# Optimization experiments

Measured on AMD Instinct MI355X. Metric: run time of the kernel, lower is better.

## Reference

```python
import jax, jax.numpy as jnp
import numpy as np

BATCH, SEQ_LEN, HIDDEN, N_TYPES = 8, 1024, 256, 4
MAX_SPAN = 12


def _span_indices(seq_len: int, max_span_length: int):
    # Enumerate (start, end) pairs in the exact order of the original triple loop:
    # start ascending, end ascending within [start, min(start+max_span, seq_len)).
    starts, ends = [], []
    for s in range(seq_len):
        for e in range(s, min(s + max_span_length, seq_len)):
            starts.append(s)
            ends.append(e)
    return np.asarray(starts, np.int32), np.asarray(ends, np.int32)


def setup_inputs() -> dict:
    key = jax.random.key(0)
    k1, k2, k3 = jax.random.split(key, 3)
    hidden_states = jax.random.normal(k1, (BATCH, SEQ_LEN, HIDDEN), dtype=jnp.float32)
    # Stacked nn.Linear(2H -> H) weights for each entity type: W[t] has shape [H, 2H]
    W = jax.random.normal(k2, (N_TYPES, HIDDEN, 2 * HIDDEN), dtype=jnp.float32) * 0.02
    b = jax.random.normal(k3, (N_TYPES, HIDDEN), dtype=jnp.float32) * 0.02
    return {"hidden_states": hidden_states, "W": W, "b": b, "max_span_length": MAX_SPAN}


def reference(hidden_states, W, b, max_span_length):
    B, S, H = hidden_states.shape
    T = W.shape[0]
    start_idx, end_idx = _span_indices(S, int(max_span_length))  # [N]
    N = start_idx.shape[0]
    h_start = hidden_states[:, start_idx, :]          # [B, N, H]
    h_end = hidden_states[:, end_idx, :]              # [B, N, H]
    cat = jnp.concatenate([h_start, h_end], axis=-1)  # [B, N, 2H]
    # Per-type linear: y = x @ W_t^T + b_t, entity type is the innermost stacking axis
    out = jnp.einsum('bnc,thc->bnth', cat, W) + b     # [B, N, T, H]
    return out.reshape(B, N * T, H)
```

## Files before the change

kernel.cpp:

```cpp
#include <hip/hip_runtime.h>
#include <hip/hip_bf16.h>
#include <cstdint>
#include <cstddef>

#define BATCH   8
#define SEQLEN  1024
#define HIDDEN  256
#define NTYPES  4
#define NSPAN   12222
#define NFULL   12156
#define NPAD    12288
#define KDIM    512
#define NCOL    1024

typedef __bf16 bf16x8 __attribute__((ext_vector_type(8)));
typedef float  f32x4  __attribute__((ext_vector_type(4)));

#define AS1 __attribute__((address_space(1)))
#define AS3 __attribute__((address_space(3)))

__device__ __forceinline__ void load16(const __bf16* g, __bf16* l) {
    __builtin_amdgcn_global_load_lds((AS1 const void*)g, (AS3 void*)l, 16, 0, 0);
}

__global__ void cvt_bf16(const float* __restrict__ src, __bf16* __restrict__ dst, int n) {
    int i = (blockIdx.x * 256 + threadIdx.x) * 4;
    if (i + 3 < n) {
        float4 f = *(const float4*)(src + i);
        struct alignas(8) B4 { __bf16 a, b, c, d; };
        B4 v;
        v.a = (__bf16)f.x; v.b = (__bf16)f.y; v.c = (__bf16)f.z; v.d = (__bf16)f.w;
        *(B4*)(dst + i) = v;
    }
}

__global__ void mk_idx(int* __restrict__ sA, int* __restrict__ eA) {
    int n = blockIdx.x * 256 + threadIdx.x;
    if (n >= NPAD) return;
    int s = 0, e = 0;
    if (n < NFULL) {
        s = n / 12;
        e = s + (n - s * 12);
    } else if (n < NSPAN) {
        int r = n - NFULL;
        s = SEQLEN - 11;
        int cnt = 11;
        while (r >= cnt) { r -= cnt; --cnt; ++s; }
        e = s + r;
    }
    sA[n] = s; eA[n] = e;
}

__global__ __launch_bounds__(256) void span_gemm(
    const __bf16* __restrict__ Hbf,
    const __bf16* __restrict__ Wbf,
    const int*    __restrict__ idxS,
    const int*    __restrict__ idxE,
    const float*  __restrict__ bias,
    float*        __restrict__ out)
{
    __shared__ alignas(16) __bf16 As[128 * 32];
    __shared__ alignas(16) __bf16 Bs[128 * 32];

    const int tid  = threadIdx.x;
    const int wave = tid >> 6;
    const int lane = tid & 63;
    const int wm   = (wave >> 1) * 64;
    const int wn   = (wave & 1) * 64;
    const int lr   = lane & 15;
    const int lq   = lane >> 4;

    const int j0 = blockIdx.x * 128;
    const int n0 = blockIdx.y * 128;
    const int b  = blockIdx.z;

    const int l0  = wave * 1024 + lane * 8;
    const int l1  = l0 + 512;
    const int mm0 = l0 >> 5, kk0 = l0 & 31;
    const int mm1 = l1 >> 5, kk1 = l1 & 31;

    const int s0 = idxS[n0 + mm0], e0 = idxE[n0 + mm0];
    const int s1 = idxS[n0 + mm1], e1 = idxE[n0 + mm1];

    const __bf16* hb = Hbf + (size_t)b * (SEQLEN * HIDDEN);
    const __bf16* w0 = Wbf + (size_t)(j0 + mm0) * KDIM + kk0;
    const __bf16* w1 = Wbf + (size_t)(j0 + mm1) * KDIM + kk1;

    f32x4 acc[4][4];
#pragma unroll
    for (int i = 0; i < 4; ++i)
#pragma unroll
        for (int j = 0; j < 4; ++j)
            acc[i][j] = (f32x4){0.f, 0.f, 0.f, 0.f};

    for (int half = 0; half < 2; ++half) {
        const __bf16* a0  = hb + (half ? e0 : s0) * HIDDEN + kk0;
        const __bf16* a1  = hb + (half ? e1 : s1) * HIDDEN + kk1;
        const __bf16* wb0 = w0 + half * HIDDEN;
        const __bf16* wb1 = w1 + half * HIDDEN;

        for (int ks = 0; ks < 8; ++ks) {
            const int c0 = ks * 32;
            __syncthreads();
            load16(a0  + c0, &As[l0]);
            load16(a1  + c0, &As[l1]);
            load16(wb0 + c0, &Bs[l0]);
            load16(wb1 + c0, &Bs[l1]);
            __syncthreads();

            bf16x8 af[4], bfv[4];
#pragma unroll
            for (int mi = 0; mi < 4; ++mi)
                af[mi] = *(const bf16x8*)(As + (wm + mi * 16 + lr) * 32 + lq * 8);
#pragma unroll
            for (int ni = 0; ni < 4; ++ni)
                bfv[ni] = *(const bf16x8*)(Bs + (wn + ni * 16 + lr) * 32 + lq * 8);
#pragma unroll
            for (int mi = 0; mi < 4; ++mi)
#pragma unroll
                for (int ni = 0; ni < 4; ++ni)
                    acc[mi][ni] = __builtin_amdgcn_mfma_f32_16x16x32_bf16(
                        af[mi], bfv[ni], acc[mi][ni], 0, 0, 0);
        }
    }

    float bv[4];
#pragma unroll
    for (int ni = 0; ni < 4; ++ni) bv[ni] = bias[j0 + wn + ni * 16 + lr];

    const size_t obase = (size_t)b * NSPAN * NCOL;
#pragma unroll
    for (int mi = 0; mi < 4; ++mi) {
#pragma unroll
        for (int r = 0; r < 4; ++r) {
            const int n = n0 + wm + mi * 16 + lq * 4 + r;
            if (n < NSPAN) {
                float* op = out + obase + (size_t)n * NCOL + (j0 + wn + lr);
#pragma unroll
                for (int ni = 0; ni < 4; ++ni)
                    op[ni * 16] = acc[mi][ni][r] + bv[ni];
            }
        }
    }
}

extern "C" void kernel_launch(void* const* d_in, const int* in_sizes, int n_in,
                              void* d_out, int out_size, void* d_ws, size_t ws_size,
                              hipStream_t stream) {
    const float* hid  = (const float*)d_in[0];
    const float* W    = (const float*)d_in[1];
    const float* bias = (const float*)d_in[2];
    float* out = (float*)d_out;

    char* ws = (char*)d_ws;
    __bf16* Wbf = (__bf16*)ws;
    __bf16* Hbf = (__bf16*)(ws + (size_t)1048576);
    int* idxS = (int*)(ws + (size_t)(1048576 + 4194304));
    int* idxE = idxS + NPAD;

    cvt_bf16<<<512,  256, 0, stream>>>(W,   Wbf, NCOL * KDIM);
    cvt_bf16<<<2048, 256, 0, stream>>>(hid, Hbf, BATCH * SEQLEN * HIDDEN);
    mk_idx<<<NPAD / 256, 256, 0, stream>>>(idxS, idxE);
    span_gemm<<<dim3(8, 96, BATCH), 256, 0, stream>>>(Hbf, Wbf, idxS, idxE, bias, out);
}
```

Measured before the change: 465.5 us.

## Factor span linear into per-token start/end projections plus gather-add

Instead of running a GEMM over all spans with a concatenated K of 512, the linear is split into start and end halves, each computed once per token (8192 rows) into an fp32 workspace PQ. A second kernel then gathers P[start] + Q[end] + bias for each span and writes the output. This removes roughly 12x redundant matmul FLOPs, at the cost of an extra 64MB fp32 intermediate written and reread. The workspace must be large enough to hold it.

```diff
diff --git a/kernel.cpp b/kernel.cpp
--- a/kernel.cpp
+++ b/kernel.cpp
@@ -6,12 +6,11 @@
 #define BATCH   8
 #define SEQLEN  1024
 #define HIDDEN  256
-#define NTYPES  4
 #define NSPAN   12222
 #define NFULL   12156
-#define NPAD    12288
 #define KDIM    512
 #define NCOL    1024
+#define NROW    8192
 
 typedef __bf16 bf16x8 __attribute__((ext_vector_type(8)));
 typedef float  f32x4  __attribute__((ext_vector_type(4)));
@@ -34,30 +33,10 @@
     }
 }
 
-__global__ void mk_idx(int* __restrict__ sA, int* __restrict__ eA) {
-    int n = blockIdx.x * 256 + threadIdx.x;
-    if (n >= NPAD) return;
-    int s = 0, e = 0;
-    if (n < NFULL) {
-        s = n / 12;
-        e = s + (n - s * 12);
-    } else if (n < NSPAN) {
-        int r = n - NFULL;
-        s = SEQLEN - 11;
-        int cnt = 11;
-        while (r >= cnt) { r -= cnt; --cnt; ++s; }
-        e = s + r;
-    }
-    sA[n] = s; eA[n] = e;
-}
-
-__global__ __launch_bounds__(256) void span_gemm(
+__global__ __launch_bounds__(256) void pq_gemm(
     const __bf16* __restrict__ Hbf,
     const __bf16* __restrict__ Wbf,
-    const int*    __restrict__ idxS,
-    const int*    __restrict__ idxE,
-    const float*  __restrict__ bias,
-    float*        __restrict__ out)
+    float*        __restrict__ PQ)
 {
     __shared__ alignas(16) __bf16 As[128 * 32];
     __shared__ alignas(16) __bf16 Bs[128 * 32];
@@ -70,21 +49,19 @@
     const int lr   = lane & 15;
     const int lq   = lane >> 4;
 
-    const int j0 = blockIdx.x * 128;
-    const int n0 = blockIdx.y * 128;
-    const int b  = blockIdx.z;
+    const int j0   = blockIdx.x * 128;
+    const int m0   = blockIdx.y * 128;
+    const int half = blockIdx.z;
 
     const int l0  = wave * 1024 + lane * 8;
     const int l1  = l0 + 512;
     const int mm0 = l0 >> 5, kk0 = l0 & 31;
     const int mm1 = l1 >> 5, kk1 = l1 & 31;
 
-    const int s0 = idxS[n0 + mm0], e0 = idxE[n0 + mm0];
-    const int s1 = idxS[n0 + mm1], e1 = idxE[n0 + mm1];
-
-    const __bf16* hb = Hbf + (size_t)b * (SEQLEN * HIDDEN);
-    const __bf16* w0 = Wbf + (size_t)(j0 + mm0) * KDIM + kk0;
-    const __bf16* w1 = Wbf + (size_t)(j0 + mm1) * KDIM + kk1;
+    const __bf16* a0 = Hbf + (size_t)(m0 + mm0) * HIDDEN + kk0;
+    const __bf16* a1 = Hbf + (size_t)(m0 + mm1) * HIDDEN + kk1;
+    const __bf16* w0 = Wbf + (size_t)(j0 + mm0) * KDIM + half * HIDDEN + kk0;
+    const __bf16* w1 = Wbf + (size_t)(j0 + mm1) * KDIM + half * HIDDEN + kk1;
 
     f32x4 acc[4][4];
 #pragma unroll
@@ -93,54 +70,81 @@
         for (int j = 0; j < 4; ++j)
             acc[i][j] = (f32x4){0.f, 0.f, 0.f, 0.f};
 
-    for (int half = 0; half < 2; ++half) {
-        const __bf16* a0  = hb + (half ? e0 : s0) * HIDDEN + kk0;
-        const __bf16* a1  = hb + (half ? e1 : s1) * HIDDEN + kk1;
-        const __bf16* wb0 = w0 + half * HIDDEN;
-        const __bf16* wb1 = w1 + half * HIDDEN;
+    for (int ks = 0; ks < 8; ++ks) {
+        const int c0 = ks * 32;
+        __syncthreads();
+        load16(a0 + c0, &As[l0]);
+        load16(a1 + c0, &As[l1]);
+        load16(w0 + c0, &Bs[l0]);
+        load16(w1 + c0, &Bs[l1]);
+        __syncthreads();
 
-        for (int ks = 0; ks < 8; ++ks) {
-            const int c0 = ks * 32;
-            __syncthreads();
-            load16(a0  + c0, &As[l0]);
-            load16(a1  + c0, &As[l1]);
-            load16(wb0 + c0, &Bs[l0]);
-            load16(wb1 + c0, &Bs[l1]);
-            __syncthreads();
-
-            bf16x8 af[4], bfv[4];
+        bf16x8 af[4], bfv[4];
 #pragma unroll
-            for (int mi = 0; mi < 4; ++mi)
-                af[mi] = *(const bf16x8*)(As + (wm + mi * 16 + lr) * 32 + lq * 8);
+        for (int mi = 0; mi < 4; ++mi)
+            af[mi] = *(const bf16x8*)(As + (wm + mi * 16 + lr) * 32 + lq * 8);
+#pragma unroll
+        for (int ni = 0; ni < 4; ++ni)
+            bfv[ni] = *(const bf16x8*)(Bs + (wn + ni * 16 + lr) * 32 + lq * 8);
+#pragma unroll
+        for (int mi = 0; mi < 4; ++mi)
 #pragma unroll
             for (int ni = 0; ni < 4; ++ni)
-                bfv[ni] = *(const bf16x8*)(Bs + (wn + ni * 16 + lr) * 32 + lq * 8);
-#pragma unroll
-            for (int mi = 0; mi < 4; ++mi)
-#pragma unroll
-                for (int ni = 0; ni < 4; ++ni)
-                    acc[mi][ni] = __builtin_amdgcn_mfma_f32_16x16x32_bf16(
-                        af[mi], bfv[ni], acc[mi][ni], 0, 0, 0);
-        }
+                acc[mi][ni] = __builtin_amdgcn_mfma_f32_16x16x32_bf16(
+                    af[mi], bfv[ni], acc[mi][ni], 0, 0, 0);
     }
 
-    float bv[4];
-#pragma unroll
-    for (int ni = 0; ni < 4; ++ni) bv[ni] = bias[j0 + wn + ni * 16 + lr];
-
-    const size_t obase = (size_t)b * NSPAN * NCOL;
+    float* base = PQ + (size_t)half * NROW * NCOL;
 #pragma unroll
     for (int mi = 0; mi < 4; ++mi) {
 #pragma unroll
         for (int r = 0; r < 4; ++r) {
-            const int n = n0 + wm + mi * 16 + lq * 4 + r;
-            if (n < NSPAN) {
-                float* op = out + obase + (size_t)n * NCOL + (j0 + wn + lr);
+            const int m = m0 + wm + mi * 16 + lq * 4 + r;
+            float* op = base + (size_t)m * NCOL + (j0 + wn + lr);
 #pragma unroll
-                for (int ni = 0; ni < 4; ++ni)
-                    op[ni * 16] = acc[mi][ni][r] + bv[ni];
-            }
+            for (int ni = 0; ni < 4; ++ni)
+                op[ni * 16] = acc[mi][ni][r];
         }
+    }
+}
+
+__global__ __launch_bounds__(256) void span_add(
+    const float* __restrict__ PQ,
+    const float* __restrict__ bias,
+    float*       __restrict__ out)
+{
+    const int b  = blockIdx.y;
+    const int n0 = blockIdx.x * 4;
+    const int j  = threadIdx.x * 4;
+
+    const float4 bv = *(const float4*)(bias + j);
+    const float* Pb = PQ + (size_t)b * SEQLEN * NCOL;
+    const float* Qb = Pb + (size_t)NROW * NCOL;
+    float* ob = out + (size_t)b * NSPAN * NCOL;
+
+#pragma unroll
+    for (int r = 0; r < 4; ++r) {
+        const int n = n0 + r;
+        if (n >= NSPAN) break;
+        int s, e;
+        if (n < NFULL) {
+            s = n / 12;
+            e = s + (n - s * 12);
+        } else {
+            int rr = n - NFULL;
+            s = SEQLEN - 11;
+            int cnt = 11;
+            while (rr >= cnt) { rr -= cnt; --cnt; ++s; }
+            e = s + rr;
+        }
+        const float4 p = *(const float4*)(Pb + (size_t)s * NCOL + j);
+        const float4 q = *(const float4*)(Qb + (size_t)e * NCOL + j);
+        float4 o;
+        o.x = p.x + q.x + bv.x;
+        o.y = p.y + q.y + bv.y;
+        o.z = p.z + q.z + bv.z;
+        o.w = p.w + q.w + bv.w;
+        *(float4*)(ob + (size_t)n * NCOL + j) = o;
     }
 }
 
@@ -155,11 +159,10 @@
     char* ws = (char*)d_ws;
     __bf16* Wbf = (__bf16*)ws;
     __bf16* Hbf = (__bf16*)(ws + (size_t)1048576);
-    int* idxS = (int*)(ws + (size_t)(1048576 + 4194304));
-    int* idxE = idxS + NPAD;
+    float*  PQ  = (float*)(ws + (size_t)(1048576 + 4194304));
 
     cvt_bf16<<<512,  256, 0, stream>>>(W,   Wbf, NCOL * KDIM);
-    cvt_bf16<<<2048, 256, 0, stream>>>(hid, Hbf, BATCH * SEQLEN * HIDDEN);
-    mk_idx<<<NPAD / 256, 256, 0, stream>>>(idxS, idxE);
-    span_gemm<<<dim3(8, 96, BATCH), 256, 0, stream>>>(Hbf, Wbf, idxS, idxE, bias, out);
+    cvt_bf16<<<2048, 256, 0, stream>>>(hid, Hbf, NROW * HIDDEN);
+    pq_gemm<<<dim3(8, 64, 2), 256, 0, stream>>>(Hbf, Wbf, PQ);
+    span_add<<<dim3((NSPAN + 3) / 4, BATCH), 256, 0, stream>>>(PQ, bias, out);
 }
```

Result: no change. 466.4 us (+0.2%).
